# Kernel optimization log

Hardware: AMD Instinct MI355X
Metric: run time of the kernel (lower is better)

The kernel has to match this reference:

```python
import jax, jax.numpy as jnp
import numpy as np

S, D = 8192, 2048      # sequence length, feature dim (input_size)
H, E, K, L = 64, 64, 2, 64  # gate hidden, expert count, top-k, expert layer_size
EPS = 1e-12            # torch F.normalize eps


def setup_inputs() -> dict:
    key = jax.random.key(0)
    ks = jax.random.split(key, 5)
    x = jax.random.normal(ks[0], (S, D), dtype=jnp.float32)
    # torch nn.Linear weights have shape [out_features, in_features]
    Wg_in = jax.random.normal(ks[1], (H, D), dtype=jnp.float32) * 0.02   # gate.input
    Wg_lin = jax.random.normal(ks[2], (E, H), dtype=jnp.float32) * 0.02  # gate.linear
    Wg_out = jax.random.normal(ks[3], (1, S), dtype=jnp.float32) * 0.02  # gate.output
    We = jax.random.normal(ks[4], (E, L, D), dtype=jnp.float32) * 0.02   # expert weight bank
    return {"x": x, "Wg_in": Wg_in, "Wg_lin": Wg_lin, "Wg_out": Wg_out, "We": We}


def reference(x, Wg_in, Wg_lin, Wg_out, We):
    # --- SparseGate (eval mode: dropout = identity) ---
    h = x @ Wg_in.T                         # [S, H]
    logits = h @ Wg_lin.T                   # [S, E]
    scores = (logits.T @ Wg_out.T)[:, 0]    # Linear(S,1) applied to [E,S] -> [E]
    topv, idx = jax.lax.top_k(scores, K)    # global top-k experts for whole input
    g = jax.nn.softmax(topv)                # softmax over the k selected logits

    # --- dispatch to k selected experts (FFNN: Linear -> normalize(-1) -> GELU) ---
    Wsel = We[idx]                          # [K, L, D]
    z = jnp.einsum('sd,kld->ksl', x, Wsel)  # [K, S, L]
    z = z / jnp.maximum(jnp.linalg.norm(z, axis=-1, keepdims=True), EPS)
    z = jax.nn.gelu(z, approximate=False)   # torch GELU default is exact erf

    # --- weighted combine: sum_k g_k * expert_k(x) ---
    return jnp.einsum('k,ksl->sl', g, z)    # [S, L]
```

## Files before the change

### kernel.cpp

```cpp
#include <hip/hip_runtime.h>
#include <hip/hip_bf16.h>
#include <math.h>

#define D_DIM 2048
#define L_DIM 64
#define E_NUM 64
#define H_DIM 64

typedef float f32x4_t __attribute__((ext_vector_type(4)));
typedef __bf16 bf16x8_t __attribute__((ext_vector_type(8)));

#define WS_UPART 0u
#define WS_META  (128u * 2048u * 4u + 2048u * 4u + 256u)
#define WS_WB    (WS_META + 64u)

__global__ __launch_bounds__(256) void k_upart(const float* __restrict__ x,
                                               const float* __restrict__ wout,
                                               float* __restrict__ upart) {
  const int d4 = (blockIdx.x * 256 + threadIdx.x) * 4;
  const int s0 = blockIdx.y * 128;
  const float* xp = x + (size_t)s0 * D_DIM + d4;
  float4 acc0 = make_float4(0.f, 0.f, 0.f, 0.f);
  float4 acc1 = make_float4(0.f, 0.f, 0.f, 0.f);
#pragma unroll 8
  for (int i = 0; i < 128; i += 2) {
    const float w0 = wout[s0 + i];
    const float w1 = wout[s0 + i + 1];
    const float4 a = *reinterpret_cast<const float4*>(xp + (size_t)i * D_DIM);
    const float4 b = *reinterpret_cast<const float4*>(xp + (size_t)(i + 1) * D_DIM);
    acc0.x += a.x * w0; acc0.y += a.y * w0; acc0.z += a.z * w0; acc0.w += a.w * w0;
    acc1.x += b.x * w1; acc1.y += b.y * w1; acc1.z += b.z * w1; acc1.w += b.w * w1;
  }
  acc0.x += acc1.x; acc0.y += acc1.y; acc0.z += acc1.z; acc0.w += acc1.w;
  *reinterpret_cast<float4*>(upart + (size_t)blockIdx.y * D_DIM + d4) = acc0;
}

__global__ __launch_bounds__(1024) void k_gate_all(
    const float* __restrict__ upart, const float* __restrict__ wg_in,
    const float* __restrict__ wg_lin, int* __restrict__ sel, float* __restrict__ g) {
  __shared__ float uS[D_DIM];
  __shared__ float vS[H_DIM];
  __shared__ float scS[E_NUM];
  const int t = threadIdx.x;
  for (int dd = t; dd < D_DIM; dd += 1024) {
    float s = 0.f;
#pragma unroll 8
    for (int c = 0; c < 64; ++c) s += upart[(size_t)c * D_DIM + dd];
    uS[dd] = s;
  }
  __syncthreads();
  const int w = t >> 6, lane = t & 63;
  for (int hh = w; hh < H_DIM; hh += 16) {
    const float4* wr = reinterpret_cast<const float4*>(wg_in + (size_t)hh * D_DIM);
    float s = 0.f;
#pragma unroll
    for (int j = 0; j < 8; ++j) {
      const float4 a = wr[lane + 64 * j];
      const float* ub = &uS[(lane + 64 * j) * 4];
      s += a.x * ub[0] + a.y * ub[1] + a.z * ub[2] + a.w * ub[3];
    }
#pragma unroll
    for (int off = 32; off; off >>= 1) s += __shfl_down(s, off, 64);
    if (lane == 0) vS[hh] = s;
  }
  __syncthreads();
  if (t < E_NUM) {
    float s = 0.f;
#pragma unroll 8
    for (int hh = 0; hh < H_DIM; ++hh) s += wg_lin[t * H_DIM + hh] * vS[hh];
    scS[t] = s;
  }
  __syncthreads();
  if (t == 0) {
    int b1 = 0; float m1 = scS[0];
    for (int e = 1; e < E_NUM; ++e) { if (scS[e] > m1) { m1 = scS[e]; b1 = e; } }
    int b2 = -1; float m2 = -3.4e38f;
    for (int e = 0; e < E_NUM; ++e) { if (e != b1 && scS[e] > m2) { m2 = scS[e]; b2 = e; } }
    const float e2 = expf(m2 - m1);
    const float g0 = 1.0f / (1.0f + e2);
    sel[0] = b1; sel[1] = b2;
    g[0] = g0; g[1] = 1.0f - g0;
  }
}

__global__ __launch_bounds__(256) void k_wb(const float* __restrict__ we,
                                            const int* __restrict__ sel,
                                            __hip_bfloat16* __restrict__ wb) {
  const int n = blockIdx.x;
  const int e = sel[n >> 6];
  const int l = n & 63;
  const float* src = we + ((size_t)e * L_DIM + l) * D_DIM;
  const int t = threadIdx.x;
  const float4 a = reinterpret_cast<const float4*>(src)[2 * t];
  const float4 b = reinterpret_cast<const float4*>(src)[2 * t + 1];
  union { __hip_bfloat16 h[8]; uint4 u; } pk;
  pk.h[0] = __float2bfloat16(a.x); pk.h[1] = __float2bfloat16(a.y);
  pk.h[2] = __float2bfloat16(a.z); pk.h[3] = __float2bfloat16(a.w);
  pk.h[4] = __float2bfloat16(b.x); pk.h[5] = __float2bfloat16(b.y);
  pk.h[6] = __float2bfloat16(b.z); pk.h[7] = __float2bfloat16(b.w);
  reinterpret_cast<uint4*>(wb + (size_t)n * D_DIM)[t] = pk.u;
}

__device__ __forceinline__ void async_ld16(const void* gp, void* lp) {
  __builtin_amdgcn_global_load_lds(
      (const __attribute__((address_space(1))) unsigned int*)gp,
      (__attribute__((address_space(3))) unsigned int*)lp, 16, 0, 0);
}

__device__ __forceinline__ float gelu_f(float v) {
  return 0.5f * v * (1.0f + erff(v * 0.70710678118654752440f));
}

#define A_OFF 0
#define B_OFF 4608
#define A_STRIDE 2304
#define B_STRIDE 16384
__global__ __launch_bounds__(256) void k_moe_gemm(
    const float* __restrict__ x, const __hip_bfloat16* __restrict__ wb,
    const float* __restrict__ gw, float* __restrict__ out) {
  __shared__ __align__(16) unsigned char lds[2 * 16 * 144 + 2 * 128 * 128];

  const int tid = threadIdx.x;
  const int wv = tid >> 6;
  const int lane = tid & 63;
  const int m0 = blockIdx.x * 16;
  const float g0 = gw[0], g1 = gw[1];

  const int ar = tid >> 4, ac = tid & 15;
  const float* gA = x + (size_t)(m0 + ar) * D_DIM + ac * 4;

  const int fr = lane & 15, fq = lane >> 4;

  f32x4_t acc0 = {0.f, 0.f, 0.f, 0.f};
  f32x4_t acc1 = acc0;

#define ISSUE_B(kk, bufo)                                                     \
  {                                                                           \
    const int k0_ = (kk) * 64;                                                \
    _Pragma("unroll") for (int i_ = 0; i_ < 4; ++i_) {                        \
      const int c_ = i_ * 256 + tid;                                          \
      const int r_ = c_ >> 3, p_ = c_ & 7;                                    \
      const int kc_ = p_ ^ (r_ & 7);                                          \
      async_ld16(wb + (size_t)r_ * D_DIM + k0_ + kc_ * 8,                     \
                 lds + B_OFF + (bufo) + c_ * 16);                             \
    }                                                                         \
  }
#define WRITE_A(av, bufo)                                                     \
  {                                                                           \
    union { __hip_bfloat16 h[4]; uint2 u; } pk_;                              \
    pk_.h[0] = __float2bfloat16((av).x); pk_.h[1] = __float2bfloat16((av).y); \
    pk_.h[2] = __float2bfloat16((av).z); pk_.h[3] = __float2bfloat16((av).w); \
    *reinterpret_cast<uint2*>(lds + A_OFF + (bufo) + ar * 144 + ac * 8) = pk_.u; \
  }

  ISSUE_B(0, 0);
  {
    const float4 a0 = *reinterpret_cast<const float4*>(gA);
    WRITE_A(a0, 0);
  }
  __syncthreads();

  for (int kk = 0; kk < 32; ++kk) {
    const int curA = (kk & 1) * A_STRIDE, nxtA = ((kk & 1) ^ 1) * A_STRIDE;
    const int curB = (kk & 1) * B_STRIDE, nxtB = ((kk & 1) ^ 1) * B_STRIDE;
    float4 aN = make_float4(0.f, 0.f, 0.f, 0.f);
    const bool more = (kk + 1) < 32;
    if (more) {
      ISSUE_B(kk + 1, nxtB);
      aN = *reinterpret_cast<const float4*>(gA + (kk + 1) * 64);
    }
    union fragu { uint4 u; bf16x8_t v; };
    fragu af[2], bfr[2][2];
#pragma unroll
    for (int ks = 0; ks < 2; ++ks)
      af[ks].u = *reinterpret_cast<const uint4*>(
          lds + A_OFF + curA + fr * 144 + ks * 64 + fq * 16);
#pragma unroll
    for (int nt = 0; nt < 2; ++nt)
#pragma unroll
      for (int ks = 0; ks < 2; ++ks) {
        const int r = wv * 32 + nt * 16 + fr;
        const int kg = ks * 4 + fq;
        bfr[nt][ks].u = *reinterpret_cast<const uint4*>(
            lds + B_OFF + curB + r * 128 + ((kg ^ (r & 7)) * 16));
      }
    acc0 = __builtin_amdgcn_mfma_f32_16x16x32_bf16(af[0].v, bfr[0][0].v, acc0, 0, 0, 0);
    acc0 = __builtin_amdgcn_mfma_f32_16x16x32_bf16(af[1].v, bfr[0][1].v, acc0, 0, 0, 0);
    acc1 = __builtin_amdgcn_mfma_f32_16x16x32_bf16(af[0].v, bfr[1][0].v, acc1, 0, 0, 0);
    acc1 = __builtin_amdgcn_mfma_f32_16x16x32_bf16(af[1].v, bfr[1][1].v, acc1, 0, 0, 0);
    if (more) WRITE_A(aN, nxtA);
    __syncthreads();
  }

  float* z = reinterpret_cast<float*>(lds);
  {
    const int colbase = wv * 32 + fr;
#pragma unroll
    for (int reg = 0; reg < 4; ++reg) {
      const int r0 = fq * 4 + reg;
      z[r0 * 132 + colbase]      = acc0[reg];
      z[r0 * 132 + colbase + 16] = acc1[reg];
    }
  }
  __syncthreads();
  float* ps = reinterpret_cast<float*>(lds + 16 * 132 * 4);
  {
    const int r = tid >> 4, seg = tid & 15;
    float s = 0.f;
#pragma unroll
    for (int i2 = 0; i2 < 8; ++i2) {
      const float t2 = z[r * 132 + seg * 8 + i2];
      s += t2 * t2;
    }
    ps[r * 16 + seg] = s;
  }
  __syncthreads();
  {
    const int r = tid >> 4, j = tid & 15;
    float s0 = 0.f, s1 = 0.f;
#pragma unroll
    for (int i2 = 0; i2 < 8; ++i2) { s0 += ps[r * 16 + i2]; s1 += ps[r * 16 + 8 + i2]; }
    const float i0 = 1.0f / fmaxf(sqrtf(s0), 1e-12f);
    const float i1 = 1.0f / fmaxf(sqrtf(s1), 1e-12f);
    float o[4];
#pragma unroll
    for (int i2 = 0; i2 < 4; ++i2) {
      const int c = j * 4 + i2;
      o[i2] = g0 * gelu_f(z[r * 132 + c] * i0) + g1 * gelu_f(z[r * 132 + 64 + c] * i1);
    }
    *reinterpret_cast<float4*>(out + (size_t)(m0 + r) * 64 + j * 4) =
        make_float4(o[0], o[1], o[2], o[3]);
  }
#undef ISSUE_B
#undef WRITE_A
}

extern "C" void kernel_launch(void* const* d_in, const int* in_sizes, int n_in,
                              void* d_out, int out_size, void* d_ws, size_t ws_size,
                              hipStream_t stream) {
  (void)in_sizes; (void)n_in; (void)out_size; (void)ws_size;
  const float* x      = (const float*)d_in[0];
  const float* wg_in  = (const float*)d_in[1];
  const float* wg_lin = (const float*)d_in[2];
  const float* wg_out = (const float*)d_in[3];
  const float* we     = (const float*)d_in[4];
  float* out = (float*)d_out;
  char* ws = (char*)d_ws;

  float* upart = (float*)(ws + WS_UPART);
  int*   sel   = (int*)(ws + WS_META);
  float* g     = (float*)(ws + WS_META + 8);
  __hip_bfloat16* wb = (__hip_bfloat16*)(ws + WS_WB);

  k_upart   <<<dim3(2, 64), 256, 0, stream>>>(x, wg_out, upart);
  k_gate_all<<<1, 1024, 0, stream>>>(upart, wg_in, wg_lin, sel, g);
  k_wb      <<<128, 256, 0, stream>>>(we, sel, wb);
  k_moe_gemm<<<512, 256, 0, stream>>>(x, wb, g, out);
}
```

Baseline: 170.8 us.

## Drop weight-conversion kernel and LDS staging; load fp32 operands directly into MFMA fragments

Removes the separate k_wb kernel that gathered and converted the selected expert weights to bf16. The GEMM now reads fp32 x and expert weights straight from global memory into registers, converts them there and feeds MFMA without any LDS staging or per-iteration barriers. Blocks grow to 512 threads covering 32 rows each, so half as many blocks are launched. The cost is uncoalesced per-lane global loads and redundant conversion work in each block, with no software prefetch to hide memory latency.

```diff
diff --git a/kernel.cpp b/kernel.cpp
--- a/kernel.cpp
+++ b/kernel.cpp
@@ -11,8 +11,8 @@
 typedef __bf16 bf16x8_t __attribute__((ext_vector_type(8)));
 
 #define WS_UPART 0u
-#define WS_META  (128u * 2048u * 4u + 2048u * 4u + 256u)
-#define WS_WB    (WS_META + 64u)
+#define WS_SEL   (64u * 2048u * 4u)
+#define WS_G     (WS_SEL + 8u)
 
 __global__ __launch_bounds__(256) void k_upart(const float* __restrict__ x,
                                                const float* __restrict__ wout,
@@ -83,127 +83,69 @@
   }
 }
 
-__global__ __launch_bounds__(256) void k_wb(const float* __restrict__ we,
-                                            const int* __restrict__ sel,
-                                            __hip_bfloat16* __restrict__ wb) {
-  const int n = blockIdx.x;
-  const int e = sel[n >> 6];
-  const int l = n & 63;
-  const float* src = we + ((size_t)e * L_DIM + l) * D_DIM;
-  const int t = threadIdx.x;
-  const float4 a = reinterpret_cast<const float4*>(src)[2 * t];
-  const float4 b = reinterpret_cast<const float4*>(src)[2 * t + 1];
-  union { __hip_bfloat16 h[8]; uint4 u; } pk;
-  pk.h[0] = __float2bfloat16(a.x); pk.h[1] = __float2bfloat16(a.y);
-  pk.h[2] = __float2bfloat16(a.z); pk.h[3] = __float2bfloat16(a.w);
-  pk.h[4] = __float2bfloat16(b.x); pk.h[5] = __float2bfloat16(b.y);
-  pk.h[6] = __float2bfloat16(b.z); pk.h[7] = __float2bfloat16(b.w);
-  reinterpret_cast<uint4*>(wb + (size_t)n * D_DIM)[t] = pk.u;
-}
-
-__device__ __forceinline__ void async_ld16(const void* gp, void* lp) {
-  __builtin_amdgcn_global_load_lds(
-      (const __attribute__((address_space(1))) unsigned int*)gp,
-      (__attribute__((address_space(3))) unsigned int*)lp, 16, 0, 0);
-}
-
 __device__ __forceinline__ float gelu_f(float v) {
   return 0.5f * v * (1.0f + erff(v * 0.70710678118654752440f));
 }
 
-#define A_OFF 0
-#define B_OFF 4608
-#define A_STRIDE 2304
-#define B_STRIDE 16384
-__global__ __launch_bounds__(256) void k_moe_gemm(
-    const float* __restrict__ x, const __hip_bfloat16* __restrict__ wb,
-    const float* __restrict__ gw, float* __restrict__ out) {
-  __shared__ __align__(16) unsigned char lds[2 * 16 * 144 + 2 * 128 * 128];
+__global__ __launch_bounds__(512) void k_moe_gemm(
+    const float* __restrict__ x, const float* __restrict__ we,
+    const int* __restrict__ sel, const float* __restrict__ gw,
+    float* __restrict__ out) {
+  const int tid = threadIdx.x;
+  const int wv = tid >> 6, lane = tid & 63;
+  const int mg = wv >> 2, ng = wv & 3;
+  const int fr = lane & 15, fq = lane >> 4;
+  const int mb = blockIdx.x * 32;
 
-  const int tid = threadIdx.x;
-  const int wv = tid >> 6;
-  const int lane = tid & 63;
-  const int m0 = blockIdx.x * 16;
-  const float g0 = gw[0], g1 = gw[1];
+  const int e = sel[ng >> 1] & 63;
+  const int l0 = (ng & 1) * 32 + fr;
 
-  const int ar = tid >> 4, ac = tid & 15;
-  const float* gA = x + (size_t)(m0 + ar) * D_DIM + ac * 4;
-
-  const int fr = lane & 15, fq = lane >> 4;
+  const float* pa  = x + (size_t)(mb + mg * 16 + fr) * D_DIM + fq * 8;
+  const float* pb0 = we + ((size_t)e * L_DIM + l0) * D_DIM + fq * 8;
+  const float* pb1 = pb0 + (size_t)16 * D_DIM;
 
   f32x4_t acc0 = {0.f, 0.f, 0.f, 0.f};
   f32x4_t acc1 = acc0;
 
-#define ISSUE_B(kk, bufo)                                                     \
-  {                                                                           \
-    const int k0_ = (kk) * 64;                                                \
-    _Pragma("unroll") for (int i_ = 0; i_ < 4; ++i_) {                        \
-      const int c_ = i_ * 256 + tid;                                          \
-      const int r_ = c_ >> 3, p_ = c_ & 7;                                    \
-      const int kc_ = p_ ^ (r_ & 7);                                          \
-      async_ld16(wb + (size_t)r_ * D_DIM + k0_ + kc_ * 8,                     \
-                 lds + B_OFF + (bufo) + c_ * 16);                             \
-    }                                                                         \
-  }
-#define WRITE_A(av, bufo)                                                     \
-  {                                                                           \
-    union { __hip_bfloat16 h[4]; uint2 u; } pk_;                              \
-    pk_.h[0] = __float2bfloat16((av).x); pk_.h[1] = __float2bfloat16((av).y); \
-    pk_.h[2] = __float2bfloat16((av).z); pk_.h[3] = __float2bfloat16((av).w); \
-    *reinterpret_cast<uint2*>(lds + A_OFF + (bufo) + ar * 144 + ac * 8) = pk_.u; \
+#pragma unroll 2
+  for (int ks = 0; ks < 64; ++ks) {
+    const int k0 = ks * 32;
+    const float4 a0 = *reinterpret_cast<const float4*>(pa + k0);
+    const float4 a1 = *reinterpret_cast<const float4*>(pa + k0 + 4);
+    const float4 b00 = *reinterpret_cast<const float4*>(pb0 + k0);
+    const float4 b01 = *reinterpret_cast<const float4*>(pb0 + k0 + 4);
+    const float4 b10 = *reinterpret_cast<const float4*>(pb1 + k0);
+    const float4 b11 = *reinterpret_cast<const float4*>(pb1 + k0 + 4);
+    union { __hip_bfloat16 h[8]; bf16x8_t v; } af, bf0, bf1;
+    af.h[0] = __float2bfloat16(a0.x);  af.h[1] = __float2bfloat16(a0.y);
+    af.h[2] = __float2bfloat16(a0.z);  af.h[3] = __float2bfloat16(a0.w);
+    af.h[4] = __float2bfloat16(a1.x);  af.h[5] = __float2bfloat16(a1.y);
+    af.h[6] = __float2bfloat16(a1.z);  af.h[7] = __float2bfloat16(a1.w);
+    bf0.h[0] = __float2bfloat16(b00.x); bf0.h[1] = __float2bfloat16(b00.y);
+    bf0.h[2] = __float2bfloat16(b00.z); bf0.h[3] = __float2bfloat16(b00.w);
+    bf0.h[4] = __float2bfloat16(b01.x); bf0.h[5] = __float2bfloat16(b01.y);
+    bf0.h[6] = __float2bfloat16(b01.z); bf0.h[7] = __float2bfloat16(b01.w);
+    bf1.h[0] = __float2bfloat16(b10.x); bf1.h[1] = __float2bfloat16(b10.y);
+    bf1.h[2] = __float2bfloat16(b10.z); bf1.h[3] = __float2bfloat16(b10.w);
+    bf1.h[4] = __float2bfloat16(b11.x); bf1.h[5] = __float2bfloat16(b11.y);
+    bf1.h[6] = __float2bfloat16(b11.z); bf1.h[7] = __float2bfloat16(b11.w);
+    acc0 = __builtin_amdgcn_mfma_f32_16x16x32_bf16(af.v, bf0.v, acc0, 0, 0, 0);
+    acc1 = __builtin_amdgcn_mfma_f32_16x16x32_bf16(af.v, bf1.v, acc1, 0, 0, 0);
   }
 
-  ISSUE_B(0, 0);
+  __shared__ __align__(16) float zs[32 * 132 + 32 * 16];
+  float* z = zs;
+  float* ps = zs + 32 * 132;
   {
-    const float4 a0 = *reinterpret_cast<const float4*>(gA);
-    WRITE_A(a0, 0);
-  }
-  __syncthreads();
-
-  for (int kk = 0; kk < 32; ++kk) {
-    const int curA = (kk & 1) * A_STRIDE, nxtA = ((kk & 1) ^ 1) * A_STRIDE;
-    const int curB = (kk & 1) * B_STRIDE, nxtB = ((kk & 1) ^ 1) * B_STRIDE;
-    float4 aN = make_float4(0.f, 0.f, 0.f, 0.f);
-    const bool more = (kk + 1) < 32;
-    if (more) {
-      ISSUE_B(kk + 1, nxtB);
-      aN = *reinterpret_cast<const float4*>(gA + (kk + 1) * 64);
-    }
-    union fragu { uint4 u; bf16x8_t v; };
-    fragu af[2], bfr[2][2];
-#pragma unroll
-    for (int ks = 0; ks < 2; ++ks)
-      af[ks].u = *reinterpret_cast<const uint4*>(
-          lds + A_OFF + curA + fr * 144 + ks * 64 + fq * 16);
-#pragma unroll
-    for (int nt = 0; nt < 2; ++nt)
-#pragma unroll
-      for (int ks = 0; ks < 2; ++ks) {
-        const int r = wv * 32 + nt * 16 + fr;
-        const int kg = ks * 4 + fq;
-        bfr[nt][ks].u = *reinterpret_cast<const uint4*>(
-            lds + B_OFF + curB + r * 128 + ((kg ^ (r & 7)) * 16));
-      }
-    acc0 = __builtin_amdgcn_mfma_f32_16x16x32_bf16(af[0].v, bfr[0][0].v, acc0, 0, 0, 0);
-    acc0 = __builtin_amdgcn_mfma_f32_16x16x32_bf16(af[1].v, bfr[0][1].v, acc0, 0, 0, 0);
-    acc1 = __builtin_amdgcn_mfma_f32_16x16x32_bf16(af[0].v, bfr[1][0].v, acc1, 0, 0, 0);
-    acc1 = __builtin_amdgcn_mfma_f32_16x16x32_bf16(af[1].v, bfr[1][1].v, acc1, 0, 0, 0);
-    if (more) WRITE_A(aN, nxtA);
-    __syncthreads();
-  }
-
-  float* z = reinterpret_cast<float*>(lds);
-  {
-    const int colbase = wv * 32 + fr;
+    const int colb = ng * 32 + fr;
+    const int rowb = mg * 16 + fq * 4;
 #pragma unroll
     for (int reg = 0; reg < 4; ++reg) {
-      const int r0 = fq * 4 + reg;
-      z[r0 * 132 + colbase]      = acc0[reg];
-      z[r0 * 132 + colbase + 16] = acc1[reg];
+      z[(rowb + reg) * 132 + colb]      = acc0[reg];
+      z[(rowb + reg) * 132 + colb + 16] = acc1[reg];
     }
   }
   __syncthreads();
-  float* ps = reinterpret_cast<float*>(lds + 16 * 132 * 4);
   {
     const int r = tid >> 4, seg = tid & 15;
     float s = 0.f;
@@ -216,6 +158,7 @@
   }
   __syncthreads();
   {
+    const float g0 = gw[0], g1 = gw[1];
     const int r = tid >> 4, j = tid & 15;
     float s0 = 0.f, s1 = 0.f;
 #pragma unroll
@@ -228,11 +171,9 @@
       const int c = j * 4 + i2;
       o[i2] = g0 * gelu_f(z[r * 132 + c] * i0) + g1 * gelu_f(z[r * 132 + 64 + c] * i1);
     }
-    *reinterpret_cast<float4*>(out + (size_t)(m0 + r) * 64 + j * 4) =
+    *reinterpret_cast<float4*>(out + (size_t)(mb + r) * 64 + j * 4) =
         make_float4(o[0], o[1], o[2], o[3]);
   }
-#undef ISSUE_B
-#undef WRITE_A
 }
 
 extern "C" void kernel_launch(void* const* d_in, const int* in_sizes, int n_in,
@@ -248,12 +189,10 @@
   char* ws = (char*)d_ws;
 
   float* upart = (float*)(ws + WS_UPART);
-  int*   sel   = (int*)(ws + WS_META);
-  float* g     = (float*)(ws + WS_META + 8);
-  __hip_bfloat16* wb = (__hip_bfloat16*)(ws + WS_WB);
+  int*   sel   = (int*)(ws + WS_SEL);
+  float* g     = (float*)(ws + WS_G);
 
   k_upart   <<<dim3(2, 64), 256, 0, stream>>>(x, wg_out, upart);
   k_gate_all<<<1, 1024, 0, stream>>>(upart, wg_in, wg_lin, sel, g);
-  k_wb      <<<128, 256, 0, stream>>>(we, sel, wb);
-  k_moe_gemm<<<512, 256, 0, stream>>>(x, wb, g, out);
+  k_moe_gemm<<<256, 512, 0, stream>>>(x, we, sel, g, out);
 }
```

Measured after the change: 227.9 us. +33.4%, slower.
